# Optimization experiments

Measured on AMD Instinct MI355X. Metric: run time of the kernel, lower is better.

Reference implementation:

```python
import jax, jax.numpy as jnp
import numpy as np

EMBED_DIM = 1024
NUM_HEADS = 16
HEAD_DIM = EMBED_DIM // NUM_HEADS
B, S = 4, 2048


def setup_inputs() -> dict:
    key = jax.random.key(0)
    ks = jax.random.split(key, 9)
    scale = 1.0 / np.sqrt(EMBED_DIM)
    inp = {
        "inputs": jax.random.normal(ks[0], (B, S, EMBED_DIM), dtype=jnp.float32),
        "rotation_params": jax.random.normal(ks[1], (B, S, EMBED_DIM), dtype=jnp.float32),
        "entangle_params": jax.random.normal(ks[2], (B, S, EMBED_DIM), dtype=jnp.float32),
        # Linear weights stored as (out, in) like torch; applied as x @ W.T
        "Wq": jax.random.normal(ks[3], (EMBED_DIM, EMBED_DIM), dtype=jnp.float32) * scale,
        "Wk": jax.random.normal(ks[4], (EMBED_DIM, EMBED_DIM), dtype=jnp.float32) * scale,
        "Wv": jax.random.normal(ks[5], (EMBED_DIM, EMBED_DIM), dtype=jnp.float32) * scale,
        "Wrot": jax.random.normal(ks[6], (EMBED_DIM, EMBED_DIM), dtype=jnp.float32) * scale,
        "Went": jax.random.normal(ks[7], (EMBED_DIM, EMBED_DIM), dtype=jnp.float32) * scale,
        "Wo": jax.random.normal(ks[8], (EMBED_DIM, EMBED_DIM), dtype=jnp.float32) * scale,
    }
    return inp


def _split_heads(x):
    b, s, e = x.shape
    return x.reshape(b, s, NUM_HEADS, HEAD_DIM).transpose(0, 2, 1, 3)  # (B,H,S,D)


def reference(inputs, rotation_params, entangle_params, Wq, Wk, Wv, Wrot, Went, Wo):
    Q = inputs @ Wq.T + rotation_params @ Wrot.T
    K = inputs @ Wk.T + entangle_params @ Went.T
    V = inputs @ Wv.T
    Qh, Kh, Vh = _split_heads(Q), _split_heads(K), _split_heads(V)
    scores = jnp.einsum("bhqd,bhkd->bhqk", Qh, Kh) / jnp.sqrt(jnp.float32(HEAD_DIM))
    attn = jax.nn.softmax(scores, axis=-1)  # dropout p=0 -> identity
    out = jnp.einsum("bhqk,bhkd->bhqd", attn, Vh)
    out = out.transpose(0, 2, 1, 3).reshape(inputs.shape[0], inputs.shape[1], EMBED_DIM)
    return out @ Wo.T
```

## Files before the change

kernel.cpp:

```cpp
#include <hip/hip_runtime.h>
#include <stdint.h>


typedef unsigned short u16;
typedef __bf16 bf16x8 __attribute__((ext_vector_type(8)));
typedef float f32x4 __attribute__((ext_vector_type(4)));
typedef float f32x16 __attribute__((ext_vector_type(16)));
typedef uint32_t u32x4 __attribute__((ext_vector_type(4)));

#define MFMA_BF16(a, b, c) __builtin_amdgcn_mfma_f32_16x16x32_bf16((a), (b), (c), 0, 0, 0)
#define MFMA32(a, b, c)    __builtin_amdgcn_mfma_f32_32x32x16_bf16((a), (b), (c), 0, 0, 0)
#define GAMMA 0.18033688011112042f
#define BHSTRIDE 131072

static __device__ __forceinline__ u16 f2bf(float f) {
    uint32_t u = __builtin_bit_cast(uint32_t, f);
    u = (u + 0x7FFFu + ((u >> 16) & 1u)) >> 16;
    return (u16)u;
}

static __device__ __forceinline__ uint32_t pk_rne2(float a, float b) {
    uint32_t ua = __builtin_bit_cast(uint32_t, a);
    uint32_t ub = __builtin_bit_cast(uint32_t, b);
    ua += 0x7FFFu + ((ua >> 16) & 1u);
    ub += 0x7FFFu + ((ub >> 16) & 1u);
    return __builtin_amdgcn_perm(ub, ua, 0x07060302);
}

static __device__ __forceinline__ void async_copy16(const void* g, void* l) {
    __builtin_amdgcn_global_load_lds((__attribute__((address_space(1))) void*)g,
                                     (__attribute__((address_space(3))) void*)l,
                                     16, 0, 0);
}

static __device__ __forceinline__ uint32_t cvtpk(float a, float b) {
    uint32_t r;
    asm("v_cvt_pk_bf16_f32 %0, %1, %2" : "=v"(r) : "v"(a), "v"(b));
    return r;
}

static __device__ __forceinline__ void plswap(uint32_t& a, uint32_t& b) {
    asm("v_permlane32_swap_b32 %0, %1" : "+v"(a), "+v"(b));
}

static __device__ __forceinline__ bf16x8 mkfrag(uint32_t w0, uint32_t w1,
                                                uint32_t w2, uint32_t w3) {
    u32x4 u = {w0, w1, w2, w3};
    return __builtin_bit_cast(bf16x8, u);
}

struct CvtArgs { const float* s[6]; u16* d[6]; };

__global__ __launch_bounds__(256) void cvt_kernel(CvtArgs a, int nelem) {
    const float* s = a.s[blockIdx.z];
    u16* d = a.d[blockIdx.z];
    int i = (blockIdx.x * 256 + threadIdx.x) * 8;
    float4 f0 = *(const float4*)(s + i);
    float4 f1 = *(const float4*)(s + i + 4);
    uint4 w;
    w.x = pk_rne2(f0.x, f0.y); w.y = pk_rne2(f0.z, f0.w);
    w.z = pk_rne2(f1.x, f1.y); w.w = pk_rne2(f1.z, f1.w);
    *(uint4*)(d + i) = w;
}

template <int AMODE, int CMODE>
__global__ __launch_bounds__(256, 2) void gemm_bt(
    const u16* __restrict__ A0, const u16* __restrict__ W0,
    const u16* __restrict__ A1, const u16* __restrict__ W1,
    void* __restrict__ Cv, int K, int npairs, float scale)
{
    __shared__ __align__(16) u16 lA[2][128 * 64];
    __shared__ __align__(16) u16 lB[2][128 * 64];

    const int tid  = threadIdx.x;
    const int lane = tid & 63;
    const int wave = tid >> 6;
    const int wm   = (wave >> 1) * 64;
    const int wn   = (wave & 1) * 64;
    const size_t m0 = (size_t)blockIdx.x * 128;
    const size_t n0 = (size_t)blockIdx.y * 128;

    const int row8 = tid >> 3;
    const int cp   = tid & 7;
    const int fr   = lane & 15;
    const int g    = lane >> 4;

    const size_t bb = (m0 >> 11) * 16;
    const size_t s0 = m0 & 2047;

    const int kpp = K >> 6;
    const int nsteps = npairs * kpp;

    f32x4 acc[4][4] = {};

    auto stage = [&](int buf, int s) {
        const u16* A = (s >= kpp) ? A1 : A0;
        const u16* W = (s >= kpp) ? W1 : W0;
        int k0 = (s >= kpp ? s - kpp : s) * 64;
#pragma unroll
        for (int it = 0; it < 4; ++it) {
            int row = it * 32 + row8;
            int sc = cp ^ (((row >> 3) ^ row) & 7);
            if (AMODE == 0) {
                async_copy16(A + ((m0 + row) * (size_t)K + k0 + sc * 8),
                             (char*)(&lA[buf][0]) + it * 4096 + tid * 16);
            } else {
                size_t base = (bb + (size_t)(k0 >> 6)) * BHSTRIDE;
                async_copy16(A + base + (s0 + row) * 64 + sc * 8,
                             (char*)(&lA[buf][0]) + it * 4096 + tid * 16);
            }
            async_copy16(W + ((n0 + row) * (size_t)K + k0 + sc * 8),
                         (char*)(&lB[buf][0]) + it * 4096 + tid * 16);
        }
    };

    stage(0, 0);
    __syncthreads();

    int cur = 0;
    for (int s = 0; s < nsteps; ++s) {
        if (s + 1 < nsteps) stage(cur ^ 1, s + 1);

        bf16x8 af[4][2], bfm[4][2];
#pragma unroll
        for (int i = 0; i < 4; ++i) {
            int row = wm + i * 16 + fr;
            int sw = ((row >> 3) ^ row) & 7;
            af[i][0] = *(const bf16x8*)(&lA[cur][0] + row * 64 + (g ^ sw) * 8);
            af[i][1] = *(const bf16x8*)(&lA[cur][0] + row * 64 + ((4 + g) ^ sw) * 8);
        }
#pragma unroll
        for (int j = 0; j < 4; ++j) {
            int row = wn + j * 16 + fr;
            int sw = ((row >> 3) ^ row) & 7;
            bfm[j][0] = *(const bf16x8*)(&lB[cur][0] + row * 64 + (g ^ sw) * 8);
            bfm[j][1] = *(const bf16x8*)(&lB[cur][0] + row * 64 + ((4 + g) ^ sw) * 8);
        }
#pragma unroll
        for (int i = 0; i < 4; ++i)
#pragma unroll
            for (int j = 0; j < 4; ++j) {
                acc[i][j] = MFMA_BF16(af[i][0], bfm[j][0], acc[i][j]);
                acc[i][j] = MFMA_BF16(af[i][1], bfm[j][1], acc[i][j]);
            }

        __syncthreads();
        cur ^= 1;
    }

#pragma unroll
    for (int i = 0; i < 4; ++i)
#pragma unroll
        for (int j = 0; j < 4; ++j) {
            if (CMODE == 2) {
                size_t row0 = m0 + wm + i * 16 + g * 4;
                size_t col  = n0 + wn + j * 16 + fr;
                size_t addr = ((row0 >> 11) * 16 + (col >> 6)) * BHSTRIDE
                            + (size_t)(col & 63) * 2048 + (row0 & 2047);
                ushort4 pk;
                pk.x = f2bf(acc[i][j][0] * scale);
                pk.y = f2bf(acc[i][j][1] * scale);
                pk.z = f2bf(acc[i][j][2] * scale);
                pk.w = f2bf(acc[i][j][3] * scale);
                *(ushort4*)((u16*)Cv + addr) = pk;
            } else {
#pragma unroll
                for (int rg = 0; rg < 4; ++rg) {
                    size_t row = m0 + wm + i * 16 + g * 4 + rg;
                    size_t col = n0 + wn + j * 16 + fr;
                    float v = acc[i][j][rg] * scale;
                    if (CMODE == 0) {
                        ((float*)Cv)[row * 1024 + col] = v;
                    } else {
                        size_t addr = ((row >> 11) * 16 + (col >> 6)) * BHSTRIDE
                                    + (row & 2047) * 64 + (col & 63);
                        ((u16*)Cv)[addr] = f2bf(v);
                    }
                }
            }
        }
}

__global__ __launch_bounds__(512, 4) void flash_kernel(
    const u16* __restrict__ Qhm, const u16* __restrict__ Khm,
    const u16* __restrict__ Vt, u16* __restrict__ Ohm)
{
    __shared__ __align__(16) u16 sK[2][128 * 64];
    __shared__ __align__(16) u16 sVt[2][64 * 128];

    const int tid  = threadIdx.x;
    const int lane = tid & 63;
    const int wave = tid >> 6;
    const int l31  = lane & 31;
    const int hg   = lane >> 5;

    const int lin  = blockIdx.x;
    const int slot = lin >> 3;
    const int bh   = (lin & 7) + 8 * (slot >> 3);
    const int q0   = (slot & 7) * 256;

    const u16* Qh = Qhm + (size_t)bh * BHSTRIDE;
    const u16* Kh = Khm + (size_t)bh * BHSTRIDE;
    const u16* Vh = Vt  + (size_t)bh * BHSTRIDE;
    u16*       Oh = Ohm + (size_t)bh * BHSTRIDE;

    bf16x8 qbf[4];
#pragma unroll
    for (int dc = 0; dc < 4; ++dc)
        qbf[dc] = *(const bf16x8*)(Qh +
            (size_t)(q0 + wave * 32 + l31) * 64 + dc * 16 + hg * 8);

    f32x16 oacc[2] = {};
    float lsum = 0.0f;

    const int krow9 = tid >> 3, kcp = tid & 7;
    const int vd5   = tid >> 4, vcp = tid & 15;

    auto stage = [&](int buf, int kt) {
#pragma unroll
        for (int it = 0; it < 2; ++it) {
            int row = it * 64 + krow9;
            int sc = kcp ^ (((row >> 3) ^ row) & 7);
            async_copy16(Kh + (size_t)(kt * 128 + row) * 64 + sc * 8,
                         (char*)(&sK[buf][0]) + it * 8192 + tid * 16);
        }
#pragma unroll
        for (int it = 0; it < 2; ++it) {
            int d = it * 32 + vd5;
            int sc = vcp ^ (d & 15);
            async_copy16(Vh + (size_t)d * 2048 + kt * 128 + sc * 8,
                         (char*)(&sVt[buf][0]) + it * 8192 + tid * 16);
        }
    };

    stage(0, 0);
    __syncthreads();

    int cur = 0;
    for (int kt = 0; kt < 16; ++kt) {
        if (kt < 15) stage(cur ^ 1, kt + 1);
        const u16* sKc = &sK[cur][0];
        const u16* sVc = &sVt[cur][0];

#pragma unroll
        for (int kc = 0; kc < 4; ++kc) {
            f32x16 sa = {};
            const int krow = kc * 32 + l31;
            const int ksw = ((krow >> 3) ^ krow) & 7;
#pragma unroll
            for (int dc = 0; dc < 4; ++dc) {
                bf16x8 ka = *(const bf16x8*)(sKc + krow * 64 + ((dc * 2 + hg) ^ ksw) * 8);
                sa = MFMA32(ka, qbf[dc], sa);
            }
            bf16x8 vb[2][2];
#pragma unroll
            for (int sub = 0; sub < 2; ++sub)
#pragma unroll
                for (int dt = 0; dt < 2; ++dt) {
                    int dr = dt * 32 + l31;
                    vb[sub][dt] = *(const bf16x8*)(sVc + dr * 128 +
                        ((kc * 4 + sub * 2 + hg) ^ (dr & 15)) * 8);
                }
            float p[16];
#pragma unroll
            for (int r = 0; r < 16; ++r) {
                p[r] = exp2f(sa[r]);
                lsum += p[r];
            }
            uint32_t w0 = cvtpk(p[0],  p[1]),  w1 = cvtpk(p[2],  p[3]);
            uint32_t w2 = cvtpk(p[4],  p[5]),  w3 = cvtpk(p[6],  p[7]);
            uint32_t w4 = cvtpk(p[8],  p[9]),  w5 = cvtpk(p[10], p[11]);
            uint32_t w6 = cvtpk(p[12], p[13]), w7 = cvtpk(p[14], p[15]);
            plswap(w0, w2); plswap(w1, w3);
            plswap(w4, w6); plswap(w5, w7);
            bf16x8 pa0 = mkfrag(w0, w1, w2, w3);
            bf16x8 pa1 = mkfrag(w4, w5, w6, w7);
            oacc[0] = MFMA32(pa0, vb[0][0], oacc[0]);
            oacc[1] = MFMA32(pa0, vb[0][1], oacc[1]);
            oacc[0] = MFMA32(pa1, vb[1][0], oacc[0]);
            oacc[1] = MFMA32(pa1, vb[1][1], oacc[1]);
        }
        __syncthreads();
        cur ^= 1;
    }

    {
        float l = lsum;
        l += __shfl_xor(l, 32);
        float inv = 1.0f / l;
#pragma unroll
        for (int r = 0; r < 16; ++r) {
            int row = (r & 3) + 4 * hg + 8 * (r >> 2);
            float invr = __shfl(inv, row);
            size_t grow = (size_t)q0 + wave * 32 + row;
            Oh[grow * 64 + l31]      = f2bf(oacc[0][r] * invr);
            Oh[grow * 64 + 32 + l31] = f2bf(oacc[1][r] * invr);
        }
    }
}

extern "C" void kernel_launch(void* const* d_in, const int* in_sizes, int n_in,
                              void* d_out, int out_size, void* d_ws, size_t ws_size,
                              hipStream_t stream)
{
    const float* X    = (const float*)d_in[0];
    const float* R    = (const float*)d_in[1];
    const float* E    = (const float*)d_in[2];
    const float* Wq   = (const float*)d_in[3];
    const float* Wk   = (const float*)d_in[4];
    const float* Wv   = (const float*)d_in[5];
    const float* Wrot = (const float*)d_in[6];
    const float* Went = (const float*)d_in[7];
    const float* Wo   = (const float*)d_in[8];

    const size_t NT = 8192 * 1024;
    const size_t NW = 1024 * 1024;

    u16* Qhm = (u16*)d_out;
    u16* Khm = Qhm + NT;
    u16* Xb  = (u16*)d_ws;
    u16* RVb = Xb + NT;
    u16* EOb = RVb + NT;
    u16* Wqb = EOb + NT;
    u16* Wkb   = Wqb + NW;
    u16* Wvb   = Wkb + NW;
    u16* Wrotb = Wvb + NW;
    u16* Wentb = Wrotb + NW;
    u16* Wob   = Wentb + NW;

    {
        CvtArgs a{};
        a.s[0] = X; a.s[1] = R; a.s[2] = E;
        a.d[0] = Xb; a.d[1] = RVb; a.d[2] = EOb;
        cvt_kernel<<<dim3(4096, 1, 3), 256, 0, stream>>>(a, (int)NT);
    }
    {
        CvtArgs a{};
        a.s[0] = Wq; a.s[1] = Wk; a.s[2] = Wv; a.s[3] = Wrot; a.s[4] = Went; a.s[5] = Wo;
        a.d[0] = Wqb; a.d[1] = Wkb; a.d[2] = Wvb; a.d[3] = Wrotb; a.d[4] = Wentb; a.d[5] = Wob;
        cvt_kernel<<<dim3(512, 1, 6), 256, 0, stream>>>(a, (int)NW);
    }

    dim3 gproj(64, 8);
    gemm_bt<0, 1><<<gproj, 256, 0, stream>>>(Xb, Wqb, RVb, Wrotb, Qhm, 1024, 2, GAMMA);
    gemm_bt<0, 1><<<gproj, 256, 0, stream>>>(Xb, Wkb, EOb, Wentb, Khm, 1024, 2, 1.0f);
    gemm_bt<0, 2><<<gproj, 256, 0, stream>>>(Xb, Wvb, nullptr, nullptr, RVb, 1024, 1, 1.0f);
    flash_kernel<<<dim3(512), 512, 0, stream>>>(Qhm, Khm, RVb, EOb);
    gemm_bt<1, 0><<<gproj, 256, 0, stream>>>(EOb, Wob, nullptr, nullptr, d_out, 1024, 1, 1.0f);
}
```

Baseline: 399.4 us.

## Single-buffer GEMM LDS and software-pipeline QK/softmax/PV in attention

The GEMM kernel drops its double-buffered LDS staging in favour of a single buffer, with a barrier before and after each tile's async copy. This halves LDS use, likely to raise occupancy, but the loads are no longer overlapped with the MFMAs. The attention kernel splits its inner loop into qk/softmax/pv helpers and interleaves two score tiles, so the exp work on one tile can overlap MFMAs on the other. It also issues the next-tile prefetch after the first two QK products, at the cost of more live registers.

```diff
diff --git a/kernel.cpp b/kernel.cpp
--- a/kernel.cpp
+++ b/kernel.cpp
@@ -69,8 +69,8 @@
     const u16* __restrict__ A1, const u16* __restrict__ W1,
     void* __restrict__ Cv, int K, int npairs, float scale)
 {
-    __shared__ __align__(16) u16 lA[2][128 * 64];
-    __shared__ __align__(16) u16 lB[2][128 * 64];
+    __shared__ __align__(16) u16 lA[128 * 64];
+    __shared__ __align__(16) u16 lB[128 * 64];
 
     const int tid  = threadIdx.x;
     const int lane = tid & 63;
@@ -88,64 +88,53 @@
     const size_t bb = (m0 >> 11) * 16;
     const size_t s0 = m0 & 2047;
 
-    const int kpp = K >> 6;
-    const int nsteps = npairs * kpp;
-
     f32x4 acc[4][4] = {};
 
-    auto stage = [&](int buf, int s) {
-        const u16* A = (s >= kpp) ? A1 : A0;
-        const u16* W = (s >= kpp) ? W1 : W0;
-        int k0 = (s >= kpp ? s - kpp : s) * 64;
-#pragma unroll
-        for (int it = 0; it < 4; ++it) {
-            int row = it * 32 + row8;
-            int sc = cp ^ (((row >> 3) ^ row) & 7);
-            if (AMODE == 0) {
-                async_copy16(A + ((m0 + row) * (size_t)K + k0 + sc * 8),
-                             (char*)(&lA[buf][0]) + it * 4096 + tid * 16);
-            } else {
-                size_t base = (bb + (size_t)(k0 >> 6)) * BHSTRIDE;
-                async_copy16(A + base + (s0 + row) * 64 + sc * 8,
-                             (char*)(&lA[buf][0]) + it * 4096 + tid * 16);
-            }
-            async_copy16(W + ((n0 + row) * (size_t)K + k0 + sc * 8),
-                         (char*)(&lB[buf][0]) + it * 4096 + tid * 16);
-        }
-    };
-
-    stage(0, 0);
-    __syncthreads();
-
-    int cur = 0;
-    for (int s = 0; s < nsteps; ++s) {
-        if (s + 1 < nsteps) stage(cur ^ 1, s + 1);
-
-        bf16x8 af[4][2], bfm[4][2];
-#pragma unroll
-        for (int i = 0; i < 4; ++i) {
-            int row = wm + i * 16 + fr;
-            int sw = ((row >> 3) ^ row) & 7;
-            af[i][0] = *(const bf16x8*)(&lA[cur][0] + row * 64 + (g ^ sw) * 8);
-            af[i][1] = *(const bf16x8*)(&lA[cur][0] + row * 64 + ((4 + g) ^ sw) * 8);
-        }
-#pragma unroll
-        for (int j = 0; j < 4; ++j) {
-            int row = wn + j * 16 + fr;
-            int sw = ((row >> 3) ^ row) & 7;
-            bfm[j][0] = *(const bf16x8*)(&lB[cur][0] + row * 64 + (g ^ sw) * 8);
-            bfm[j][1] = *(const bf16x8*)(&lB[cur][0] + row * 64 + ((4 + g) ^ sw) * 8);
-        }
-#pragma unroll
-        for (int i = 0; i < 4; ++i)
+    for (int p = 0; p < npairs; ++p) {
+        const u16* A = p ? A1 : A0;
+        const u16* W = p ? W1 : W0;
+        for (int k0 = 0; k0 < K; k0 += 64) {
+            __syncthreads();
+#pragma unroll
+            for (int it = 0; it < 4; ++it) {
+                int row = it * 32 + row8;
+                int sc = cp ^ (((row >> 3) ^ row) & 7);
+                if (AMODE == 0) {
+                    async_copy16(A + ((m0 + row) * (size_t)K + k0 + sc * 8),
+                                 (char*)lA + it * 4096 + tid * 16);
+                } else {
+                    size_t base = (bb + (size_t)(k0 >> 6)) * BHSTRIDE;
+                    async_copy16(A + base + (s0 + row) * 64 + sc * 8,
+                                 (char*)lA + it * 4096 + tid * 16);
+                }
+                async_copy16(W + ((n0 + row) * (size_t)K + k0 + sc * 8),
+                             (char*)lB + it * 4096 + tid * 16);
+            }
+            __syncthreads();
+
+            bf16x8 af[4][2], bfm[4][2];
+#pragma unroll
+            for (int i = 0; i < 4; ++i) {
+                int row = wm + i * 16 + fr;
+                int sw = ((row >> 3) ^ row) & 7;
+                af[i][0] = *(const bf16x8*)(lA + row * 64 + (g ^ sw) * 8);
+                af[i][1] = *(const bf16x8*)(lA + row * 64 + ((4 + g) ^ sw) * 8);
+            }
 #pragma unroll
             for (int j = 0; j < 4; ++j) {
-                acc[i][j] = MFMA_BF16(af[i][0], bfm[j][0], acc[i][j]);
-                acc[i][j] = MFMA_BF16(af[i][1], bfm[j][1], acc[i][j]);
-            }
-
-        __syncthreads();
-        cur ^= 1;
+                int row = wn + j * 16 + fr;
+                int sw = ((row >> 3) ^ row) & 7;
+                bfm[j][0] = *(const bf16x8*)(lB + row * 64 + (g ^ sw) * 8);
+                bfm[j][1] = *(const bf16x8*)(lB + row * 64 + ((4 + g) ^ sw) * 8);
+            }
+#pragma unroll
+            for (int i = 0; i < 4; ++i)
+#pragma unroll
+                for (int j = 0; j < 4; ++j) {
+                    acc[i][j] = MFMA_BF16(af[i][0], bfm[j][0], acc[i][j]);
+                    acc[i][j] = MFMA_BF16(af[i][1], bfm[j][1], acc[i][j]);
+                }
+        }
     }
 
 #pragma unroll
@@ -233,53 +222,69 @@
         }
     };
 
+    auto qk = [&](const u16* sKc, int kc) -> f32x16 {
+        f32x16 sa = {};
+        const int krow = kc * 32 + l31;
+        const int ksw = ((krow >> 3) ^ krow) & 7;
+#pragma unroll
+        for (int dc = 0; dc < 4; ++dc) {
+            bf16x8 ka = *(const bf16x8*)(sKc + krow * 64 + ((dc * 2 + hg) ^ ksw) * 8);
+            sa = MFMA32(ka, qbf[dc], sa);
+        }
+        return sa;
+    };
+
+    auto sm = [&](const f32x16& sa, bf16x8& o0, bf16x8& o1) {
+        float p[16];
+#pragma unroll
+        for (int r = 0; r < 16; ++r) {
+            p[r] = exp2f(sa[r]);
+            lsum += p[r];
+        }
+        uint32_t w0 = cvtpk(p[0],  p[1]),  w1 = cvtpk(p[2],  p[3]);
+        uint32_t w2 = cvtpk(p[4],  p[5]),  w3 = cvtpk(p[6],  p[7]);
+        uint32_t w4 = cvtpk(p[8],  p[9]),  w5 = cvtpk(p[10], p[11]);
+        uint32_t w6 = cvtpk(p[12], p[13]), w7 = cvtpk(p[14], p[15]);
+        plswap(w0, w2); plswap(w1, w3);
+        plswap(w4, w6); plswap(w5, w7);
+        o0 = mkfrag(w0, w1, w2, w3);
+        o1 = mkfrag(w4, w5, w6, w7);
+    };
+
+    auto pv = [&](const u16* sVc, int kc, bf16x8 pa0, bf16x8 pa1) {
+        bf16x8 vb[2][2];
+#pragma unroll
+        for (int sub = 0; sub < 2; ++sub)
+#pragma unroll
+            for (int dt = 0; dt < 2; ++dt) {
+                int dr = dt * 32 + l31;
+                vb[sub][dt] = *(const bf16x8*)(sVc + dr * 128 +
+                    ((kc * 4 + sub * 2 + hg) ^ (dr & 15)) * 8);
+            }
+        oacc[0] = MFMA32(pa0, vb[0][0], oacc[0]);
+        oacc[1] = MFMA32(pa0, vb[0][1], oacc[1]);
+        oacc[0] = MFMA32(pa1, vb[1][0], oacc[0]);
+        oacc[1] = MFMA32(pa1, vb[1][1], oacc[1]);
+    };
+
     stage(0, 0);
     __syncthreads();
 
     int cur = 0;
     for (int kt = 0; kt < 16; ++kt) {
-        if (kt < 15) stage(cur ^ 1, kt + 1);
         const u16* sKc = &sK[cur][0];
         const u16* sVc = &sVt[cur][0];
 
-#pragma unroll
-        for (int kc = 0; kc < 4; ++kc) {
-            f32x16 sa = {};
-            const int krow = kc * 32 + l31;
-            const int ksw = ((krow >> 3) ^ krow) & 7;
-#pragma unroll
-            for (int dc = 0; dc < 4; ++dc) {
-                bf16x8 ka = *(const bf16x8*)(sKc + krow * 64 + ((dc * 2 + hg) ^ ksw) * 8);
-                sa = MFMA32(ka, qbf[dc], sa);
-            }
-            bf16x8 vb[2][2];
-#pragma unroll
-            for (int sub = 0; sub < 2; ++sub)
-#pragma unroll
-                for (int dt = 0; dt < 2; ++dt) {
-                    int dr = dt * 32 + l31;
-                    vb[sub][dt] = *(const bf16x8*)(sVc + dr * 128 +
-                        ((kc * 4 + sub * 2 + hg) ^ (dr & 15)) * 8);
-                }
-            float p[16];
-#pragma unroll
-            for (int r = 0; r < 16; ++r) {
-                p[r] = exp2f(sa[r]);
-                lsum += p[r];
-            }
-            uint32_t w0 = cvtpk(p[0],  p[1]),  w1 = cvtpk(p[2],  p[3]);
-            uint32_t w2 = cvtpk(p[4],  p[5]),  w3 = cvtpk(p[6],  p[7]);
-            uint32_t w4 = cvtpk(p[8],  p[9]),  w5 = cvtpk(p[10], p[11]);
-            uint32_t w6 = cvtpk(p[12], p[13]), w7 = cvtpk(p[14], p[15]);
-            plswap(w0, w2); plswap(w1, w3);
-            plswap(w4, w6); plswap(w5, w7);
-            bf16x8 pa0 = mkfrag(w0, w1, w2, w3);
-            bf16x8 pa1 = mkfrag(w4, w5, w6, w7);
-            oacc[0] = MFMA32(pa0, vb[0][0], oacc[0]);
-            oacc[1] = MFMA32(pa0, vb[0][1], oacc[1]);
-            oacc[0] = MFMA32(pa1, vb[1][0], oacc[0]);
-            oacc[1] = MFMA32(pa1, vb[1][1], oacc[1]);
-        }
+        f32x16 saA = qk(sKc, 0);
+        f32x16 saB = qk(sKc, 1);
+        if (kt < 15) stage(cur ^ 1, kt + 1);
+
+        bf16x8 a0, a1, b0, b1;
+        sm(saA, a0, a1);  saA = qk(sKc, 2);  pv(sVc, 0, a0, a1);
+        sm(saB, b0, b1);  saB = qk(sKc, 3);  pv(sVc, 1, b0, b1);
+        sm(saA, a0, a1);                     pv(sVc, 2, a0, a1);
+        sm(saB, b0, b1);                     pv(sVc, 3, b0, b1);
+
         __syncthreads();
         cur ^= 1;
     }
```

New measurement: 397.2 us. Within noise of the previous version (-0.6%).
